# Kernel optimization log

Measured on AMD Instinct MI355X. Metric: run time of the kernel, lower is better.

The kernel has to match this reference:

```python
import jax, jax.numpy as jnp
import numpy as np

N_EXPERTS = 8
TOP_K = 2
AUX_COEF = 0.01
Z_COEF = 0.001


def setup_inputs() -> dict:
    key = jax.random.key(0)
    ks = jax.random.split(key, 5)
    B, S, D, F, E = 2, 2048, 768, 2048, N_EXPERTS
    std = 0.02
    std_out = std / np.sqrt(2 * 12)  # scale_init_by_depth, n_layers=12
    return {
        "x": jax.random.normal(ks[0], (B, S, D), jnp.float32),
        "router_w": jax.random.normal(ks[1], (D, E), jnp.float32) * std,
        "w1": jax.random.normal(ks[2], (E, D, F), jnp.float32) * std,
        "w2": jax.random.normal(ks[3], (E, F, D), jnp.float32) * std_out,
        "w3": jax.random.normal(ks[4], (E, D, F), jnp.float32) * std,
    }


def reference(x, router_w, w1, w2, w3):
    B, S, D = x.shape
    E = w1.shape[0]
    x_flat = x.reshape(-1, D)                      # [N, D]
    n_tokens = x_flat.shape[0]

    router_logits = x_flat @ router_w               # [N, E]
    probs = jax.nn.softmax(router_logits.astype(jnp.float32), axis=-1)
    topk_w, topk_i = jax.lax.top_k(probs, TOP_K)    # [N, K]
    topk_w = topk_w / jnp.sum(topk_w, axis=-1, keepdims=True)

    # Combine: equivalent to sort/group dispatch + per-expert GEMM + index_add,
    # expressed as a masked per-expert (fixed, small E) dense pass.
    out = jnp.zeros((n_tokens, D), dtype=x.dtype)
    for e in range(E):
        gate = jnp.sum(jnp.where(topk_i == e, topk_w, 0.0), axis=-1)  # [N] f32
        h = jax.nn.silu(x_flat @ w1[e]) * (x_flat @ w3[e])            # [N, F]
        out = out + gate[:, None].astype(x.dtype) * (h @ w2[e])

    # Switch-style load-balancing aux loss + z-loss
    importance = probs.mean(axis=0)                 # [E]
    top1 = topk_i[:, 0]
    load = jnp.zeros((E,), jnp.float32).at[top1].add(1.0) / n_tokens
    aux_loss = E * jnp.sum(importance * load) * AUX_COEF
    z_loss = jnp.mean(router_logits.astype(jnp.float32) ** 2) * Z_COEF

    return out.reshape(B, S, D), aux_loss, z_loss
```

## Files before the change

kernel.cpp:

```cpp
#include <hip/hip_runtime.h>
#include <hip/hip_bf16.h>

constexpr int NT = 4096;
constexpr int DD = 768;
constexpr int FF = 2048;
constexpr int NE = 8;
constexpr int MAXROWS = 9216;
constexpr int MAXMT128 = 72;
constexpr int MAXMT256 = 40;
constexpr int NKT1 = DD / 64;

constexpr int IDX_CNTA   = 0;
constexpr int IDX_CNTT1  = 8;
constexpr int IDX_CUR    = 16;
constexpr int IDX_IMP    = 24;
constexpr int IDX_ZSUM   = 32;
constexpr int IDX_NTILES = 33;
constexpr int IDX_OFF    = 34;
constexpr int IDX_EXPT   = 48;
constexpr int IDX_N256   = 120;
constexpr int IDX_E256   = 128;
constexpr int IDX_B256   = 168;
constexpr int IDX_L256   = 208;

constexpr size_t OFF_META   = 0;
constexpr size_t OFF_TKE    = 1024;
constexpr size_t OFF_GATE   = OFF_TKE    + (size_t)NT*2*4;
constexpr size_t OFF_ROWOF  = OFF_GATE   + (size_t)NT*2*4;
constexpr size_t OFF_TOKROW = OFF_ROWOF  + (size_t)NT*2*4;
constexpr size_t OFF_XG     = 136192;
constexpr size_t OFF_W1T    = OFF_XG  + (size_t)MAXROWS*DD*2;
constexpr size_t OFF_W3T    = OFF_W1T + (size_t)NE*FF*DD*2;
constexpr size_t OFF_W2T    = OFF_W3T + (size_t)NE*FF*DD*2;
constexpr size_t OFF_H      = OFF_W2T + (size_t)NE*FF*DD*2;
constexpr size_t OFF_OP     = OFF_H   + (size_t)MAXROWS*FF*2;

typedef float f32x4 __attribute__((ext_vector_type(4)));
typedef __bf16 bf16x8v __attribute__((ext_vector_type(8)));
typedef unsigned short u16x8 __attribute__((ext_vector_type(8)));

__device__ inline unsigned short f2bf_bits(float f) {
  __bf16 h = (__bf16)f;
  return *(unsigned short*)&h;
}
__device__ inline float bf2f(unsigned short u) {
  unsigned v = (unsigned)u << 16;
  return *(float*)&v;
}

__device__ __forceinline__ void glds16(const void* g, void* l) {
  __builtin_amdgcn_global_load_lds(
      (const __attribute__((address_space(1))) unsigned int*)g,
      (__attribute__((address_space(3))) unsigned int*)l, 16, 0, 0);
}

constexpr int RB = 128;
__global__ __launch_bounds__(256) void router_kernel(const float* __restrict__ x,
    const float* __restrict__ rw, int* __restrict__ meta,
    int* __restrict__ tke, float* __restrict__ gateArr) {
  __shared__ float s_imp[NE];
  __shared__ float s_z;
  __shared__ int s_cnt1[NE], s_cnta[NE];
  if (threadIdx.x < NE) { s_imp[threadIdx.x] = 0.f; s_cnt1[threadIdx.x] = 0; s_cnta[threadIdx.x] = 0; }
  if (threadIdx.x == 0) s_z = 0.f;
  __syncthreads();

  const int wave = threadIdx.x >> 6, lane = threadIdx.x & 63;
  float impacc[NE];
  #pragma unroll
  for (int e = 0; e < NE; ++e) impacc[e] = 0.f;
  float zacc = 0.f;

  for (int t = blockIdx.x * 4 + wave; t < NT; t += RB * 4) {
    float acc[NE];
    #pragma unroll
    for (int e = 0; e < NE; ++e) acc[e] = 0.f;
    const float* xr = x + (size_t)t * DD;
    for (int i = lane; i < DD; i += 64) {
      float xv = xr[i];
      const float* r = rw + i * NE;
      #pragma unroll
      for (int e = 0; e < NE; ++e) acc[e] += xv * r[e];
    }
    #pragma unroll
    for (int off = 32; off > 0; off >>= 1) {
      #pragma unroll
      for (int e = 0; e < NE; ++e) acc[e] += __shfl_xor(acc[e], off);
    }
    float mx = acc[0];
    #pragma unroll
    for (int e = 1; e < NE; ++e) mx = fmaxf(mx, acc[e]);
    float p[NE]; float s = 0.f;
    #pragma unroll
    for (int e = 0; e < NE; ++e) { p[e] = __expf(acc[e] - mx); s += p[e]; }
    float inv = 1.f / s;
    #pragma unroll
    for (int e = 0; e < NE; ++e) p[e] *= inv;
    int e0 = 0; float p0 = p[0];
    #pragma unroll
    for (int e = 1; e < NE; ++e) if (p[e] > p0) { p0 = p[e]; e0 = e; }
    int e1 = -1; float p1 = -1.f;
    #pragma unroll
    for (int e = 0; e < NE; ++e) if (e != e0 && p[e] > p1) { p1 = p[e]; e1 = e; }
    if (lane == 0) {
      #pragma unroll
      for (int e = 0; e < NE; ++e) { impacc[e] += p[e]; zacc += acc[e] * acc[e]; }
      atomicAdd(&s_cnt1[e0], 1);
      atomicAdd(&s_cnta[e0], 1);
      atomicAdd(&s_cnta[e1], 1);
      float gs = 1.f / (p0 + p1);
      tke[t*2]   = e0; tke[t*2+1] = e1;
      gateArr[t*2] = p0 * gs; gateArr[t*2+1] = p1 * gs;
    }
  }
  if (lane == 0) {
    #pragma unroll
    for (int e = 0; e < NE; ++e) atomicAdd(&s_imp[e], impacc[e]);
    atomicAdd(&s_z, zacc);
  }
  __syncthreads();
  float* fmeta = (float*)meta;
  if (threadIdx.x < NE) {
    atomicAdd(&fmeta[IDX_IMP + threadIdx.x], s_imp[threadIdx.x]);
    atomicAdd(&meta[IDX_CNTT1 + threadIdx.x], s_cnt1[threadIdx.x]);
    atomicAdd(&meta[IDX_CNTA + threadIdx.x], s_cnta[threadIdx.x]);
  }
  if (threadIdx.x == NE) atomicAdd(&fmeta[IDX_ZSUM], s_z);
}

__global__ __launch_bounds__(128) void scan_kernel(int* __restrict__ meta,
                                                   float* __restrict__ out_tail) {
  __shared__ int s_off[NE + 1];
  __shared__ int s_nt[NE];
  __shared__ float s_aux;
  const int t = threadIdx.x;
  if (t < NE) s_nt[t] = (meta[IDX_CNTA + t] + 127) >> 7;
  __syncthreads();
  if (t == 0) {
    int off = 0;
    for (int e = 0; e < NE; ++e) { s_off[e] = off; off += s_nt[e]; }
    s_off[NE] = off;
  }
  __syncthreads();
  const int ntiles = s_off[NE];
  if (t < NE) meta[IDX_OFF + t] = s_off[t] << 7;
  if (t == NE) { meta[IDX_OFF + NE] = ntiles << 7; meta[IDX_NTILES] = ntiles; }
  if (t < ntiles) {
    int e = 0;
    while (t >= s_off[e + 1]) e++;
    meta[IDX_EXPT + t] = e;
  }
  if (t == 0) {
    int n2t = 0;
    for (int e = 0; e < NE; ++e) {
      const int base = s_off[e] << 7;
      const int lim  = base + (s_nt[e] << 7);
      const int n2 = (s_nt[e] + 1) >> 1;
      for (int i = 0; i < n2; ++i) {
        meta[IDX_E256 + n2t] = e;
        meta[IDX_B256 + n2t] = base + (i << 8);
        meta[IDX_L256 + n2t] = lim;
        ++n2t;
      }
    }
    meta[IDX_N256] = n2t;
  }
  float* fmeta = (float*)meta;
  float pl = 0.f;
  if (t < NE)
    pl = (fmeta[IDX_IMP + t] / (float)NT) * ((float)meta[IDX_CNTT1 + t] / (float)NT);
  if (t < 64) {
    #pragma unroll
    for (int off = 4; off > 0; off >>= 1) pl += __shfl_xor(pl, off);
    if (t == 0) s_aux = pl;
  }
  __syncthreads();
  if (t == 0) {
    out_tail[0] = (float)NE * s_aux * 0.01f;
    out_tail[1] = fmeta[IDX_ZSUM] / (float)(NT * NE) * 0.001f;
  }
}

__global__ __launch_bounds__(256) void scatter_kernel(const int* __restrict__ tke,
    int* __restrict__ meta, int* __restrict__ rowof, int* __restrict__ tokrow) {
  __shared__ int s_cnt[NE], s_base[NE];
  const int t = blockIdx.x * 256 + threadIdx.x;
  if (threadIdx.x < NE) s_cnt[threadIdx.x] = 0;
  __syncthreads();
  const int e0 = tke[t*2], e1 = tke[t*2 + 1];
  const int l0 = atomicAdd(&s_cnt[e0], 1);
  const int l1 = atomicAdd(&s_cnt[e1], 1);
  __syncthreads();
  if (threadIdx.x < NE)
    s_base[threadIdx.x] = atomicAdd(&meta[IDX_CUR + threadIdx.x], s_cnt[threadIdx.x]);
  __syncthreads();
  const int r0 = meta[IDX_OFF + e0] + s_base[e0] + l0;
  const int r1 = meta[IDX_OFF + e1] + s_base[e1] + l1;
  rowof[t*2]     = r0;
  rowof[t*2 + 1] = r1;
  tokrow[r0] = t;
  tokrow[r1] = t;
}

__global__ __launch_bounds__(192) void gather_kernel(const float* __restrict__ x,
    const int* __restrict__ tokrow, const int* __restrict__ meta,
    __bf16* __restrict__ Xg) {
  const int row = blockIdx.x;
  if (row >= meta[IDX_OFF + NE]) return;
  const int tok = tokrow[row];
  ushort4* dst = (ushort4*)(Xg + (size_t)row * DD);
  const int i = threadIdx.x;
  ushort4 o;
  if (tok >= 0) {
    float4 v = ((const float4*)(x + (size_t)tok * DD))[i];
    o.x = f2bf_bits(v.x); o.y = f2bf_bits(v.y);
    o.z = f2bf_bits(v.z); o.w = f2bf_bits(v.w);
  } else {
    o.x = o.y = o.z = o.w = 0;
  }
  dst[i] = o;
}

constexpr int TS = 68;
__global__ __launch_bounds__(256) void transpose_cvt_all(
    const float* __restrict__ w1, const float* __restrict__ w3,
    const float* __restrict__ w2, __bf16* __restrict__ W1t,
    __bf16* __restrict__ W3t, __bf16* __restrict__ W2t) {
  const int z = blockIdx.z, which = z >> 3, e = z & 7;
  const float* src; __bf16* dst; int R, C, rt, ct;
  if (which == 0)      { src = w1; dst = W1t; R = DD; C = FF; rt = blockIdx.y; ct = blockIdx.x; }
  else if (which == 1) { src = w3; dst = W3t; R = DD; C = FF; rt = blockIdx.y; ct = blockIdx.x; }
  else                 { src = w2; dst = W2t; R = FF; C = DD; rt = blockIdx.x; ct = blockIdx.y; }
  src += (size_t)e * DD * FF; dst += (size_t)e * DD * FF;
  const int r0 = rt * 64, c0 = ct * 64;
  __shared__ __align__(16) __bf16 tile[64 * TS];
  const int t = threadIdx.x;
  #pragma unroll
  for (int i = 0; i < 4; ++i) {
    int idx = t + i * 256; int r = idx >> 4, q = idx & 15;
    float4 v = *(const float4*)&src[(size_t)(r0 + r) * C + c0 + q * 4];
    ushort4 o;
    o.x = f2bf_bits(v.x); o.y = f2bf_bits(v.y);
    o.z = f2bf_bits(v.z); o.w = f2bf_bits(v.w);
    *(ushort4*)&tile[r * TS + q * 4] = o;
  }
  __syncthreads();
  #pragma unroll
  for (int i = 0; i < 2; ++i) {
    int idx = t + i * 256; int c = idx >> 3, seg = idx & 7;
    u16x8 o;
    #pragma unroll
    for (int k = 0; k < 8; ++k)
      o[k] = *(unsigned short*)&tile[(seg * 8 + k) * TS + c];
    *(u16x8*)&dst[(size_t)(c0 + c) * R + r0 + seg * 8] = o;
  }
}

__global__ __launch_bounds__(512, 2) void gemm1_kernel(
    const __bf16* __restrict__ Xg, const __bf16* __restrict__ W1t,
    const __bf16* __restrict__ W3t, __bf16* __restrict__ Hb,
    const int* __restrict__ meta) {
  const int wgRaw = blockIdx.x + (int)gridDim.x * blockIdx.y;
  const int wg = (wgRaw & 7) * 80 + (wgRaw >> 3);
  const int mt = wg >> 4;
  const int n0 = (wg & 15) * 128;
  if (mt >= meta[IDX_N256]) return;
  const int e      = meta[IDX_E256 + mt];
  const int m0     = meta[IDX_B256 + mt];
  const int rowlim = meta[IDX_L256 + mt];

  __shared__ __align__(16) __bf16 As[2][256 * 64];
  __shared__ __align__(16) __bf16 Bs[2][256 * 64];

  const int t = threadIdx.x, lane = t & 63, wid = t >> 6;
  const int wm = wid >> 2, wn = wid & 3;
  const int lane15 = lane & 15, g = lane >> 4;

  const __bf16* __restrict__ W1e = W1t + (size_t)e * FF * DD;
  const __bf16* __restrict__ W3e = W3t + (size_t)e * FF * DD;

  const int aBase = (wm * 128 + lane15) * 64;
  const int bBase = (wn * 64 + lane15) * 64;
  const int c0 = ((g    ) ^ (lane & 7)) * 8;
  const int c1 = ((4 + g) ^ (lane & 7)) * 8;

  const int o0v = t, o1v = 512 + t;
  const int r0v = o0v >> 3, r1v = o1v >> 3;
  const int cl0 = (o0v & 7) ^ (r0v & 7), cl1 = (o1v & 7) ^ (r1v & 7);
  int gA00 = m0 + r0v;        if (gA00 >= MAXROWS) gA00 = 0;
  int gA01 = m0 + r1v;        if (gA01 >= MAXROWS) gA01 = 0;
  int gA10 = m0 + 128 + r0v;  if (gA10 >= MAXROWS) gA10 = 0;
  int gA11 = m0 + 128 + r1v;  if (gA11 >= MAXROWS) gA11 = 0;
  const __bf16* aS00 = Xg + (size_t)gA00 * DD + cl0 * 8;
  const __bf16* aS01 = Xg + (size_t)gA01 * DD + cl1 * 8;
  const __bf16* aS10 = Xg + (size_t)gA10 * DD + cl0 * 8;
  const __bf16* aS11 = Xg + (size_t)gA11 * DD + cl1 * 8;
  const int fc0 = n0 + ((r0v >> 5) << 4) + (r0v & 15);
  const int fc1 = n0 + ((r1v >> 5) << 4) + (r1v & 15);
  const __bf16* bW0 = (r0v & 16) ? W3e : W1e;
  const __bf16* bW1 = (r1v & 16) ? W3e : W1e;
  const __bf16* bS00 = bW0 + (size_t)fc0 * DD + cl0 * 8;
  const __bf16* bS01 = bW1 + (size_t)fc1 * DD + cl1 * 8;
  const __bf16* bS10 = bW0 + (size_t)(fc0 + 64) * DD + cl0 * 8;
  const __bf16* bS11 = bW1 + (size_t)(fc1 + 64) * DD + cl1 * 8;
  const int L00 = (       wid * 64) * 8;
  const int L01 = ( 512 + wid * 64) * 8;
  const int L10 = (1024 + wid * 64) * 8;
  const int L11 = (1536 + wid * 64) * 8;

  auto st2 = [&](__bf16* dstBuf, int kt, const __bf16* s0, const __bf16* s1,
                 int d0, int d1) {
    glds16(s0 + (size_t)kt * 64, dstBuf + d0);
    glds16(s1 + (size_t)kt * 64, dstBuf + d1);
  };

  const f32x4 zero = {0.f, 0.f, 0.f, 0.f};
  f32x4 acc[8][4];
  #pragma unroll
  for (int i = 0; i < 8; ++i)
    #pragma unroll
    for (int j = 0; j < 4; ++j) acc[i][j] = zero;

  __bf16 *Ac = &As[0][0], *An = &As[1][0];
  __bf16 *Bc = &Bs[0][0], *Bn = &Bs[1][0];

  st2(Ac, 0, aS00, aS01, L00, L01); st2(Ac, 0, aS10, aS11, L10, L11);
  st2(Bc, 0, bS00, bS01, L00, L01); st2(Bc, 0, bS10, bS11, L10, L11);
  st2(An, 1, aS00, aS01, L00, L01); st2(An, 1, aS10, aS11, L10, L11);
  st2(Bn, 1, bS00, bS01, L00, L01); st2(Bn, 1, bS10, bS11, L10, L11);
  asm volatile("s_waitcnt vmcnt(8)" ::: "memory");
  __builtin_amdgcn_s_barrier();

  bf16x8v af[8], ag[8], bf[8];

  for (int k = 0; k < NKT1; ++k) {
    const bool k2ok = (k < NKT1 - 2);
    #pragma unroll
    for (int i = 0; i < 4; ++i) {
      af[i*2+0] = *(const bf16x8v*)&Ac[aBase + i*1024 + c0];
      af[i*2+1] = *(const bf16x8v*)&Ac[aBase + i*1024 + c1];
    }
    #pragma unroll
    for (int j = 0; j < 4; ++j) {
      bf[j*2+0] = *(const bf16x8v*)&Bc[bBase + j*1024 + c0];
      bf[j*2+1] = *(const bf16x8v*)&Bc[bBase + j*1024 + c1];
    }
    __builtin_amdgcn_s_barrier();
    asm volatile("s_waitcnt lgkmcnt(0)" ::: "memory");
    __builtin_amdgcn_s_setprio(1);
    #pragma unroll
    for (int i = 0; i < 4; ++i)
      #pragma unroll
      for (int j = 0; j < 2; ++j) {
        acc[i][j] = __builtin_amdgcn_mfma_f32_16x16x32_bf16(af[i*2+0], bf[j*2+0], acc[i][j], 0, 0, 0);
        acc[i][j] = __builtin_amdgcn_mfma_f32_16x16x32_bf16(af[i*2+1], bf[j*2+1], acc[i][j], 0, 0, 0);
      }
    __builtin_amdgcn_s_setprio(0);
    __builtin_amdgcn_s_barrier();

    #pragma unroll
    for (int i = 0; i < 4; ++i) {
      ag[i*2+0] = *(const bf16x8v*)&Ac[aBase + (4+i)*1024 + c0];
      ag[i*2+1] = *(const bf16x8v*)&Ac[aBase + (4+i)*1024 + c1];
    }
    if (k2ok) st2(Bc, k + 2, bS00, bS01, L00, L01);
    __builtin_amdgcn_s_barrier();
    asm volatile("s_waitcnt lgkmcnt(0)" ::: "memory");
    __builtin_amdgcn_s_setprio(1);
    #pragma unroll
    for (int i = 0; i < 4; ++i)
      #pragma unroll
      for (int j = 0; j < 2; ++j) {
        acc[4+i][j] = __builtin_amdgcn_mfma_f32_16x16x32_bf16(ag[i*2+0], bf[j*2+0], acc[4+i][j], 0, 0, 0);
        acc[4+i][j] = __builtin_amdgcn_mfma_f32_16x16x32_bf16(ag[i*2+1], bf[j*2+1], acc[4+i][j], 0, 0, 0);
      }
    __builtin_amdgcn_s_setprio(0);
    __builtin_amdgcn_s_barrier();

    if (k2ok) {
      st2(Ac, k + 2, aS00, aS01, L00, L01);
      st2(Bc, k + 2, bS10, bS11, L10, L11);
    }
    __builtin_amdgcn_s_barrier();
    __builtin_amdgcn_s_setprio(1);
    #pragma unroll
    for (int i = 0; i < 4; ++i)
      #pragma unroll
      for (int j = 0; j < 2; ++j) {
        acc[i][2+j] = __builtin_amdgcn_mfma_f32_16x16x32_bf16(af[i*2+0], bf[(2+j)*2+0], acc[i][2+j], 0, 0, 0);
        acc[i][2+j] = __builtin_amdgcn_mfma_f32_16x16x32_bf16(af[i*2+1], bf[(2+j)*2+1], acc[i][2+j], 0, 0, 0);
      }
    __builtin_amdgcn_s_setprio(0);
    __builtin_amdgcn_s_barrier();

    if (k2ok) st2(Ac, k + 2, aS10, aS11, L10, L11);
    __builtin_amdgcn_s_barrier();
    __builtin_amdgcn_s_setprio(1);
    #pragma unroll
    for (int i = 0; i < 4; ++i)
      #pragma unroll
      for (int j = 0; j < 2; ++j) {
        acc[4+i][2+j] = __builtin_amdgcn_mfma_f32_16x16x32_bf16(ag[i*2+0], bf[(2+j)*2+0], acc[4+i][2+j], 0, 0, 0);
        acc[4+i][2+j] = __builtin_amdgcn_mfma_f32_16x16x32_bf16(ag[i*2+1], bf[(2+j)*2+1], acc[4+i][2+j], 0, 0, 0);
      }
    __builtin_amdgcn_s_setprio(0);
    if (k2ok)               { asm volatile("s_waitcnt vmcnt(8)" ::: "memory"); }
    else if (k == NKT1 - 2) { asm volatile("s_waitcnt vmcnt(0)" ::: "memory"); }
    __builtin_amdgcn_s_barrier();

    __bf16* tp;
    tp = Ac; Ac = An; An = tp;
    tp = Bc; Bc = Bn; Bn = tp;
  }

  #pragma unroll
  for (int i = 0; i < 8; ++i) {
    const int grow = m0 + wm * 128 + i * 16 + (lane >> 4) * 4;
    #pragma unroll
    for (int p = 0; p < 2; ++p) {
      const int col = n0 + (wn * 2 + p) * 16 + lane15;
      const f32x4 v1 = acc[i][2*p], v3 = acc[i][2*p + 1];
      #pragma unroll
      for (int r = 0; r < 4; ++r) {
        if (grow + r < rowlim) {
          float h = v1[r] / (1.f + __expf(-v1[r])) * v3[r];
          Hb[(size_t)(grow + r) * FF + col] = (__bf16)h;
        }
      }
    }
  }
}

__global__ __launch_bounds__(256) void gemm2_kernel(const __bf16* __restrict__ Hb,
    const __bf16* __restrict__ W2t, __bf16* __restrict__ OP,
    const int* __restrict__ meta) {
  const int mt = blockIdx.y;
  if (mt >= meta[IDX_NTILES]) return;
  const int e = meta[IDX_EXPT + mt];
  const int n0 = blockIdx.x * 128;
  const int m0 = mt * 128;
  __shared__ __align__(16) __bf16 As[128*32], Bs[128*32];
  const int t = threadIdx.x, wave = t >> 6, lane = t & 63;
  const int wm = wave & 1, wn = wave >> 1;
  const __bf16* w2e = W2t + (size_t)e * DD * FF;
  const f32x4 zero = {0.f, 0.f, 0.f, 0.f};
  f32x4 acc[4][4];
  #pragma unroll
  for (int i = 0; i < 4; ++i)
    #pragma unroll
    for (int j = 0; j < 4; ++j) acc[i][j] = zero;

  const __bf16* gA = Hb  + (size_t)(m0 + 32*wave + (lane >> 2)) * FF + (lane & 3) * 8;
  const __bf16* gB = w2e + (size_t)(n0 + 32*wave + (lane >> 2)) * FF + (lane & 3) * 8;
  __bf16* lA0 = &As[(32*wave     ) * 32];
  __bf16* lA1 = &As[(32*wave + 16) * 32];
  __bf16* lB0 = &Bs[(32*wave     ) * 32];
  __bf16* lB1 = &Bs[(32*wave + 16) * 32];

  for (int k0 = 0; k0 < FF; k0 += 32) {
    glds16(gA + k0,          lA0);
    glds16(gA + k0 + 16*FF,  lA1);
    glds16(gB + k0,          lB0);
    glds16(gB + k0 + 16*FF,  lB1);
    __syncthreads();
    bf16x8v a[4], b[4];
    #pragma unroll
    for (int i = 0; i < 4; ++i) {
      a[i] = *(const bf16x8v*)&As[(64*wm + 16*i + (lane & 15))*32 + (lane >> 4)*8];
      b[i] = *(const bf16x8v*)&Bs[(64*wn + 16*i + (lane & 15))*32 + (lane >> 4)*8];
    }
    #pragma unroll
    for (int i = 0; i < 4; ++i)
      #pragma unroll
      for (int j = 0; j < 4; ++j)
        acc[i][j] = __builtin_amdgcn_mfma_f32_16x16x32_bf16(a[i], b[j], acc[i][j], 0, 0, 0);
    __syncthreads();
  }
  #pragma unroll
  for (int i = 0; i < 4; ++i) {
    const int rowb = m0 + 64*wm + 16*i + (lane >> 4)*4;
    #pragma unroll
    for (int j = 0; j < 4; ++j) {
      const int col = n0 + 64*wn + 16*j + (lane & 15);
      #pragma unroll
      for (int r = 0; r < 4; ++r)
        OP[(size_t)(rowb + r)*DD + col] = (__bf16)acc[i][j][r];
    }
  }
}

__global__ __launch_bounds__(192) void combine_kernel(const __bf16* __restrict__ OP,
    const int* __restrict__ rowof, const float* __restrict__ gateArr,
    float* __restrict__ out) {
  const int t = blockIdx.x;
  const int r0 = rowof[t*2], r1 = rowof[t*2 + 1];
  const float g0 = gateArr[t*2], g1 = gateArr[t*2 + 1];
  const ushort4* p0 = (const ushort4*)(OP + (size_t)r0 * DD);
  const ushort4* p1 = (const ushort4*)(OP + (size_t)r1 * DD);
  const int i = threadIdx.x;
  ushort4 a = p0[i], b = p1[i];
  float4 o;
  o.x = g0 * bf2f(a.x) + g1 * bf2f(b.x);
  o.y = g0 * bf2f(a.y) + g1 * bf2f(b.y);
  o.z = g0 * bf2f(a.z) + g1 * bf2f(b.z);
  o.w = g0 * bf2f(a.w) + g1 * bf2f(b.w);
  ((float4*)(out + (size_t)t * DD))[i] = o;
}

extern "C" void kernel_launch(void* const* d_in, const int* in_sizes, int n_in,
                              void* d_out, int out_size, void* d_ws, size_t ws_size,
                              hipStream_t stream) {
  const float* x  = (const float*)d_in[0];
  const float* rw = (const float*)d_in[1];
  const float* w1 = (const float*)d_in[2];
  const float* w2 = (const float*)d_in[3];
  const float* w3 = (const float*)d_in[4];
  float* out = (float*)d_out;

  char* ws = (char*)d_ws;
  int*    meta   = (int*)(ws + OFF_META);
  int*    tke    = (int*)(ws + OFF_TKE);
  float*  gateA  = (float*)(ws + OFF_GATE);
  int*    rowof  = (int*)(ws + OFF_ROWOF);
  int*    tokrow = (int*)(ws + OFF_TOKROW);
  __bf16* Xg     = (__bf16*)(ws + OFF_XG);
  __bf16* W1t    = (__bf16*)(ws + OFF_W1T);
  __bf16* W3t    = (__bf16*)(ws + OFF_W3T);
  __bf16* W2t    = (__bf16*)(ws + OFF_W2T);
  __bf16* Hb     = (__bf16*)(ws + OFF_H);
  __bf16* OP     = (__bf16*)(ws + OFF_OP);

  hipMemsetAsync(ws + OFF_META, 0, 1024, stream);
  hipMemsetAsync(ws + OFF_TOKROW, 0xFF, (size_t)MAXROWS * 4, stream);

  transpose_cvt_all<<<dim3(32, 12, 24), 256, 0, stream>>>(w1, w3, w2, W1t, W3t, W2t);

  router_kernel<<<RB, 256, 0, stream>>>(x, rw, meta, tke, gateA);
  scan_kernel<<<1, 128, 0, stream>>>(meta, out + (size_t)NT * DD);
  scatter_kernel<<<NT/256, 256, 0, stream>>>(tke, meta, rowof, tokrow);
  gather_kernel<<<MAXROWS, 192, 0, stream>>>(x, tokrow, meta, Xg);

  gemm1_kernel<<<dim3(FF/128, MAXMT256), 512, 0, stream>>>(Xg, W1t, W3t, Hb, meta);
  gemm2_kernel<<<dim3(DD/128, MAXMT128), 256, 0, stream>>>(Hb, W2t, OP, meta);
  combine_kernel<<<NT, 192, 0, stream>>>(OP, rowof, gateA, out);
}
```

Baseline: 393.1 us.

## Make gemm1 persistent with atomic work-queue tile scheduling

```diff
diff --git a/kernel.cpp b/kernel.cpp
--- a/kernel.cpp
+++ b/kernel.cpp
@@ -22,6 +22,7 @@
 constexpr int IDX_E256   = 128;
 constexpr int IDX_B256   = 168;
 constexpr int IDX_L256   = 208;
+constexpr int IDX_WORK   = 250;
 
 constexpr size_t OFF_META   = 0;
 constexpr size_t OFF_TKE    = 1024;
@@ -259,172 +260,185 @@
 __global__ __launch_bounds__(512, 2) void gemm1_kernel(
     const __bf16* __restrict__ Xg, const __bf16* __restrict__ W1t,
     const __bf16* __restrict__ W3t, __bf16* __restrict__ Hb,
-    const int* __restrict__ meta) {
-  const int wgRaw = blockIdx.x + (int)gridDim.x * blockIdx.y;
-  const int wg = (wgRaw & 7) * 80 + (wgRaw >> 3);
-  const int mt = wg >> 4;
-  const int n0 = (wg & 15) * 128;
-  if (mt >= meta[IDX_N256]) return;
-  const int e      = meta[IDX_E256 + mt];
-  const int m0     = meta[IDX_B256 + mt];
-  const int rowlim = meta[IDX_L256 + mt];
-
+    int* __restrict__ meta) {
   __shared__ __align__(16) __bf16 As[2][256 * 64];
   __shared__ __align__(16) __bf16 Bs[2][256 * 64];
+  __shared__ int s_wi;
 
   const int t = threadIdx.x, lane = t & 63, wid = t >> 6;
   const int wm = wid >> 2, wn = wid & 3;
   const int lane15 = lane & 15, g = lane >> 4;
 
-  const __bf16* __restrict__ W1e = W1t + (size_t)e * FF * DD;
-  const __bf16* __restrict__ W3e = W3t + (size_t)e * FF * DD;
-
   const int aBase = (wm * 128 + lane15) * 64;
-  const int bBase = (wn * 64 + lane15) * 64;
+  const int bBase = (wn * 32 + lane15) * 64;
   const int c0 = ((g    ) ^ (lane & 7)) * 8;
   const int c1 = ((4 + g) ^ (lane & 7)) * 8;
 
   const int o0v = t, o1v = 512 + t;
   const int r0v = o0v >> 3, r1v = o1v >> 3;
   const int cl0 = (o0v & 7) ^ (r0v & 7), cl1 = (o1v & 7) ^ (r1v & 7);
-  int gA00 = m0 + r0v;        if (gA00 >= MAXROWS) gA00 = 0;
-  int gA01 = m0 + r1v;        if (gA01 >= MAXROWS) gA01 = 0;
-  int gA10 = m0 + 128 + r0v;  if (gA10 >= MAXROWS) gA10 = 0;
-  int gA11 = m0 + 128 + r1v;  if (gA11 >= MAXROWS) gA11 = 0;
-  const __bf16* aS00 = Xg + (size_t)gA00 * DD + cl0 * 8;
-  const __bf16* aS01 = Xg + (size_t)gA01 * DD + cl1 * 8;
-  const __bf16* aS10 = Xg + (size_t)gA10 * DD + cl0 * 8;
-  const __bf16* aS11 = Xg + (size_t)gA11 * DD + cl1 * 8;
-  const int fc0 = n0 + ((r0v >> 5) << 4) + (r0v & 15);
-  const int fc1 = n0 + ((r1v >> 5) << 4) + (r1v & 15);
-  const __bf16* bW0 = (r0v & 16) ? W3e : W1e;
-  const __bf16* bW1 = (r1v & 16) ? W3e : W1e;
-  const __bf16* bS00 = bW0 + (size_t)fc0 * DD + cl0 * 8;
-  const __bf16* bS01 = bW1 + (size_t)fc1 * DD + cl1 * 8;
-  const __bf16* bS10 = bW0 + (size_t)(fc0 + 64) * DD + cl0 * 8;
-  const __bf16* bS11 = bW1 + (size_t)(fc1 + 64) * DD + cl1 * 8;
   const int L00 = (       wid * 64) * 8;
   const int L01 = ( 512 + wid * 64) * 8;
   const int L10 = (1024 + wid * 64) * 8;
   const int L11 = (1536 + wid * 64) * 8;
-
-  auto st2 = [&](__bf16* dstBuf, int kt, const __bf16* s0, const __bf16* s1,
-                 int d0, int d1) {
-    glds16(s0 + (size_t)kt * 64, dstBuf + d0);
-    glds16(s1 + (size_t)kt * 64, dstBuf + d1);
-  };
-
-  const f32x4 zero = {0.f, 0.f, 0.f, 0.f};
-  f32x4 acc[8][4];
-  #pragma unroll
-  for (int i = 0; i < 8; ++i)
-    #pragma unroll
-    for (int j = 0; j < 4; ++j) acc[i][j] = zero;
-
-  __bf16 *Ac = &As[0][0], *An = &As[1][0];
-  __bf16 *Bc = &Bs[0][0], *Bn = &Bs[1][0];
-
-  st2(Ac, 0, aS00, aS01, L00, L01); st2(Ac, 0, aS10, aS11, L10, L11);
-  st2(Bc, 0, bS00, bS01, L00, L01); st2(Bc, 0, bS10, bS11, L10, L11);
-  st2(An, 1, aS00, aS01, L00, L01); st2(An, 1, aS10, aS11, L10, L11);
-  st2(Bn, 1, bS00, bS01, L00, L01); st2(Bn, 1, bS10, bS11, L10, L11);
-  asm volatile("s_waitcnt vmcnt(8)" ::: "memory");
-  __builtin_amdgcn_s_barrier();
-
-  bf16x8v af[8], ag[8], bf[8];
-
-  for (int k = 0; k < NKT1; ++k) {
-    const bool k2ok = (k < NKT1 - 2);
-    #pragma unroll
-    for (int i = 0; i < 4; ++i) {
-      af[i*2+0] = *(const bf16x8v*)&Ac[aBase + i*1024 + c0];
-      af[i*2+1] = *(const bf16x8v*)&Ac[aBase + i*1024 + c1];
-    }
-    #pragma unroll
-    for (int j = 0; j < 4; ++j) {
-      bf[j*2+0] = *(const bf16x8v*)&Bc[bBase + j*1024 + c0];
-      bf[j*2+1] = *(const bf16x8v*)&Bc[bBase + j*1024 + c1];
-    }
+  const int fcb0 = ((r0v >> 5) << 4) + (r0v & 15);
+  const int fcb1 = ((r1v >> 5) << 4) + (r1v & 15);
+  const bool w3sel0 = (r0v & 16) != 0, w3sel1 = (r1v & 16) != 0;
+
+  const int nItems = meta[IDX_N256] * 16;
+
+  while (true) {
+    if (t == 0) s_wi = atomicAdd(&meta[IDX_WORK], 1);
+    __syncthreads();
+    const int wi = s_wi;
+    if (wi >= nItems) return;
+    const int mt = wi >> 4;
+    const int n0 = (wi & 15) * 128;
+    const int e      = meta[IDX_E256 + mt];
+    const int m0     = meta[IDX_B256 + mt];
+    const int rowlim = meta[IDX_L256 + mt];
+
+    const __bf16* __restrict__ W1e = W1t + (size_t)e * FF * DD;
+    const __bf16* __restrict__ W3e = W3t + (size_t)e * FF * DD;
+
+    int gA00 = m0 + r0v;        if (gA00 >= MAXROWS) gA00 = 0;
+    int gA01 = m0 + r1v;        if (gA01 >= MAXROWS) gA01 = 0;
+    int gA10 = m0 + 128 + r0v;  if (gA10 >= MAXROWS) gA10 = 0;
+    int gA11 = m0 + 128 + r1v;  if (gA11 >= MAXROWS) gA11 = 0;
+    const __bf16* aS00 = Xg + (size_t)gA00 * DD + cl0 * 8;
+    const __bf16* aS01 = Xg + (size_t)gA01 * DD + cl1 * 8;
+    const __bf16* aS10 = Xg + (size_t)gA10 * DD + cl0 * 8;
+    const __bf16* aS11 = Xg + (size_t)gA11 * DD + cl1 * 8;
+    const __bf16* bW0 = w3sel0 ? W3e : W1e;
+    const __bf16* bW1 = w3sel1 ? W3e : W1e;
+    const __bf16* bS00 = bW0 + (size_t)(n0 + fcb0) * DD + cl0 * 8;
+    const __bf16* bS01 = bW1 + (size_t)(n0 + fcb1) * DD + cl1 * 8;
+    const __bf16* bS10 = bW0 + (size_t)(n0 + fcb0 + 64) * DD + cl0 * 8;
+    const __bf16* bS11 = bW1 + (size_t)(n0 + fcb1 + 64) * DD + cl1 * 8;
+
+    auto st2 = [&](__bf16* dstBuf, int kt, const __bf16* s0, const __bf16* s1,
+                   int d0, int d1) {
+      glds16(s0 + (size_t)kt * 64, dstBuf + d0);
+      glds16(s1 + (size_t)kt * 64, dstBuf + d1);
+    };
+
+    const f32x4 zero = {0.f, 0.f, 0.f, 0.f};
+    f32x4 acc[8][4];
+    #pragma unroll
+    for (int i = 0; i < 8; ++i)
+      #pragma unroll
+      for (int j = 0; j < 4; ++j) acc[i][j] = zero;
+
+    __bf16 *Ac = &As[0][0], *An = &As[1][0];
+    __bf16 *Bc = &Bs[0][0], *Bn = &Bs[1][0];
+
+    st2(Ac, 0, aS00, aS01, L00, L01); st2(Ac, 0, aS10, aS11, L10, L11);
+    st2(Bc, 0, bS00, bS01, L00, L01); st2(Bc, 0, bS10, bS11, L10, L11);
+    st2(An, 1, aS00, aS01, L00, L01); st2(An, 1, aS10, aS11, L10, L11);
+    st2(Bn, 1, bS00, bS01, L00, L01); st2(Bn, 1, bS10, bS11, L10, L11);
+    asm volatile("s_waitcnt vmcnt(8)" ::: "memory");
     __builtin_amdgcn_s_barrier();
-    asm volatile("s_waitcnt lgkmcnt(0)" ::: "memory");
-    __builtin_amdgcn_s_setprio(1);
-    #pragma unroll
-    for (int i = 0; i < 4; ++i)
+
+    bf16x8v af[8], ag[8], bfr[8];
+
+    for (int k = 0; k < NKT1; ++k) {
+      const bool k2ok = (k < NKT1 - 2);
+      #pragma unroll
+      for (int i = 0; i < 4; ++i) {
+        af[i*2+0] = *(const bf16x8v*)&Ac[aBase + i*1024 + c0];
+        af[i*2+1] = *(const bf16x8v*)&Ac[aBase + i*1024 + c1];
+      }
       #pragma unroll
       for (int j = 0; j < 2; ++j) {
-        acc[i][j] = __builtin_amdgcn_mfma_f32_16x16x32_bf16(af[i*2+0], bf[j*2+0], acc[i][j], 0, 0, 0);
-        acc[i][j] = __builtin_amdgcn_mfma_f32_16x16x32_bf16(af[i*2+1], bf[j*2+1], acc[i][j], 0, 0, 0);
-      }
-    __builtin_amdgcn_s_setprio(0);
-    __builtin_amdgcn_s_barrier();
-
-    #pragma unroll
-    for (int i = 0; i < 4; ++i) {
-      ag[i*2+0] = *(const bf16x8v*)&Ac[aBase + (4+i)*1024 + c0];
-      ag[i*2+1] = *(const bf16x8v*)&Ac[aBase + (4+i)*1024 + c1];
-    }
-    if (k2ok) st2(Bc, k + 2, bS00, bS01, L00, L01);
-    __builtin_amdgcn_s_barrier();
-    asm volatile("s_waitcnt lgkmcnt(0)" ::: "memory");
-    __builtin_amdgcn_s_setprio(1);
-    #pragma unroll
-    for (int i = 0; i < 4; ++i)
+        bfr[j*2+0] = *(const bf16x8v*)&Bc[bBase + j*1024 + c0];
+        bfr[j*2+1] = *(const bf16x8v*)&Bc[bBase + j*1024 + c1];
+      }
+      __builtin_amdgcn_s_barrier();
+      asm volatile("s_waitcnt lgkmcnt(0)" ::: "memory");
+      __builtin_amdgcn_s_setprio(1);
+      #pragma unroll
+      for (int i = 0; i < 4; ++i)
+        #pragma unroll
+        for (int j = 0; j < 2; ++j) {
+          acc[i][j] = __builtin_amdgcn_mfma_f32_16x16x32_bf16(af[i*2+0], bfr[j*2+0], acc[i][j], 0, 0, 0);
+          acc[i][j] = __builtin_amdgcn_mfma_f32_16x16x32_bf16(af[i*2+1], bfr[j*2+1], acc[i][j], 0, 0, 0);
+        }
+      __builtin_amdgcn_s_setprio(0);
+      __builtin_amdgcn_s_barrier();
+
+      #pragma unroll
+      for (int i = 0; i < 4; ++i) {
+        ag[i*2+0] = *(const bf16x8v*)&Ac[aBase + (4+i)*1024 + c0];
+        ag[i*2+1] = *(const bf16x8v*)&Ac[aBase + (4+i)*1024 + c1];
+      }
       #pragma unroll
       for (int j = 0; j < 2; ++j) {
-        acc[4+i][j] = __builtin_amdgcn_mfma_f32_16x16x32_bf16(ag[i*2+0], bf[j*2+0], acc[4+i][j], 0, 0, 0);
-        acc[4+i][j] = __builtin_amdgcn_mfma_f32_16x16x32_bf16(ag[i*2+1], bf[j*2+1], acc[4+i][j], 0, 0, 0);
-      }
-    __builtin_amdgcn_s_setprio(0);
-    __builtin_amdgcn_s_barrier();
-
-    if (k2ok) {
-      st2(Ac, k + 2, aS00, aS01, L00, L01);
-      st2(Bc, k + 2, bS10, bS11, L10, L11);
-    }
-    __builtin_amdgcn_s_barrier();
-    __builtin_amdgcn_s_setprio(1);
-    #pragma unroll
-    for (int i = 0; i < 4; ++i)
-      #pragma unroll
-      for (int j = 0; j < 2; ++j) {
-        acc[i][2+j] = __builtin_amdgcn_mfma_f32_16x16x32_bf16(af[i*2+0], bf[(2+j)*2+0], acc[i][2+j], 0, 0, 0);
-        acc[i][2+j] = __builtin_amdgcn_mfma_f32_16x16x32_bf16(af[i*2+1], bf[(2+j)*2+1], acc[i][2+j], 0, 0, 0);
-      }
-    __builtin_amdgcn_s_setprio(0);
-    __builtin_amdgcn_s_barrier();
-
-    if (k2ok) st2(Ac, k + 2, aS10, aS11, L10, L11);
-    __builtin_amdgcn_s_barrier();
-    __builtin_amdgcn_s_setprio(1);
-    #pragma unroll
-    for (int i = 0; i < 4; ++i)
-      #pragma unroll
-      for (int j = 0; j < 2; ++j) {
-        acc[4+i][2+j] = __builtin_amdgcn_mfma_f32_16x16x32_bf16(ag[i*2+0], bf[(2+j)*2+0], acc[4+i][2+j], 0, 0, 0);
-        acc[4+i][2+j] = __builtin_amdgcn_mfma_f32_16x16x32_bf16(ag[i*2+1], bf[(2+j)*2+1], acc[4+i][2+j], 0, 0, 0);
-      }
-    __builtin_amdgcn_s_setprio(0);
-    if (k2ok)               { asm volatile("s_waitcnt vmcnt(8)" ::: "memory"); }
-    else if (k == NKT1 - 2) { asm volatile("s_waitcnt vmcnt(0)" ::: "memory"); }
-    __builtin_amdgcn_s_barrier();
-
-    __bf16* tp;
-    tp = Ac; Ac = An; An = tp;
-    tp = Bc; Bc = Bn; Bn = tp;
-  }
-
-  #pragma unroll
-  for (int i = 0; i < 8; ++i) {
-    const int grow = m0 + wm * 128 + i * 16 + (lane >> 4) * 4;
-    #pragma unroll
-    for (int p = 0; p < 2; ++p) {
-      const int col = n0 + (wn * 2 + p) * 16 + lane15;
-      const f32x4 v1 = acc[i][2*p], v3 = acc[i][2*p + 1];
-      #pragma unroll
-      for (int r = 0; r < 4; ++r) {
-        if (grow + r < rowlim) {
-          float h = v1[r] / (1.f + __expf(-v1[r])) * v3[r];
-          Hb[(size_t)(grow + r) * FF + col] = (__bf16)h;
+        bfr[4+j*2+0] = *(const bf16x8v*)&Bc[bBase + 8192 + j*1024 + c0];
+        bfr[4+j*2+1] = *(const bf16x8v*)&Bc[bBase + 8192 + j*1024 + c1];
+      }
+      if (k2ok) st2(Bc, k + 2, bS00, bS01, L00, L01);
+      __builtin_amdgcn_s_barrier();
+      asm volatile("s_waitcnt lgkmcnt(0)" ::: "memory");
+      __builtin_amdgcn_s_setprio(1);
+      #pragma unroll
+      for (int i = 0; i < 4; ++i)
+        #pragma unroll
+        for (int j = 0; j < 2; ++j) {
+          acc[4+i][j] = __builtin_amdgcn_mfma_f32_16x16x32_bf16(ag[i*2+0], bfr[j*2+0], acc[4+i][j], 0, 0, 0);
+          acc[4+i][j] = __builtin_amdgcn_mfma_f32_16x16x32_bf16(ag[i*2+1], bfr[j*2+1], acc[4+i][j], 0, 0, 0);
+        }
+      __builtin_amdgcn_s_setprio(0);
+      __builtin_amdgcn_s_barrier();
+
+      if (k2ok) {
+        st2(Ac, k + 2, aS00, aS01, L00, L01);
+        st2(Bc, k + 2, bS10, bS11, L10, L11);
+      }
+      __builtin_amdgcn_s_barrier();
+      __builtin_amdgcn_s_setprio(1);
+      #pragma unroll
+      for (int i = 0; i < 4; ++i)
+        #pragma unroll
+        for (int j = 0; j < 2; ++j) {
+          acc[i][2+j] = __builtin_amdgcn_mfma_f32_16x16x32_bf16(af[i*2+0], bfr[4+j*2+0], acc[i][2+j], 0, 0, 0);
+          acc[i][2+j] = __builtin_amdgcn_mfma_f32_16x16x32_bf16(af[i*2+1], bfr[4+j*2+1], acc[i][2+j], 0, 0, 0);
+        }
+      __builtin_amdgcn_s_setprio(0);
+      __builtin_amdgcn_s_barrier();
+
+      if (k2ok) st2(Ac, k + 2, aS10, aS11, L10, L11);
+      __builtin_amdgcn_s_barrier();
+      __builtin_amdgcn_s_setprio(1);
+      #pragma unroll
+      for (int i = 0; i < 4; ++i)
+        #pragma unroll
+        for (int j = 0; j < 2; ++j) {
+          acc[4+i][2+j] = __builtin_amdgcn_mfma_f32_16x16x32_bf16(ag[i*2+0], bfr[4+j*2+0], acc[4+i][2+j], 0, 0, 0);
+          acc[4+i][2+j] = __builtin_amdgcn_mfma_f32_16x16x32_bf16(ag[i*2+1], bfr[4+j*2+1], acc[4+i][2+j], 0, 0, 0);
+        }
+      __builtin_amdgcn_s_setprio(0);
+      if (k2ok)               { asm volatile("s_waitcnt vmcnt(8)" ::: "memory"); }
+      else if (k == NKT1 - 2) { asm volatile("s_waitcnt vmcnt(0)" ::: "memory"); }
+      __builtin_amdgcn_s_barrier();
+
+      __bf16* tp;
+      tp = Ac; Ac = An; An = tp;
+      tp = Bc; Bc = Bn; Bn = tp;
+    }
+
+    #pragma unroll
+    for (int i = 0; i < 8; ++i) {
+      const int grow = m0 + wm * 128 + i * 16 + (lane >> 4) * 4;
+      #pragma unroll
+      for (int p = 0; p < 2; ++p) {
+        const int col = n0 + (wn + p * 4) * 16 + lane15;
+        const f32x4 v1 = acc[i][2*p], v3 = acc[i][2*p + 1];
+        #pragma unroll
+        for (int r = 0; r < 4; ++r) {
+          if (grow + r < rowlim) {
+            float h = v1[r] / (1.f + __expf(-v1[r])) * v3[r];
+            Hb[(size_t)(grow + r) * FF + col] = (__bf16)h;
+          }
         }
       }
     }
@@ -540,7 +554,7 @@
   scatter_kernel<<<NT/256, 256, 0, stream>>>(tke, meta, rowof, tokrow);
   gather_kernel<<<MAXROWS, 192, 0, stream>>>(x, tokrow, meta, Xg);
 
-  gemm1_kernel<<<dim3(FF/128, MAXMT256), 512, 0, stream>>>(Xg, W1t, W3t, Hb, meta);
+  gemm1_kernel<<<dim3(256), 512, 0, stream>>>(Xg, W1t, W3t, Hb, meta);
   gemm2_kernel<<<dim3(DD/128, MAXMT128), 256, 0, stream>>>(Hb, W2t, OP, meta);
   combine_kernel<<<NT, 192, 0, stream>>>(OP, rowof, gateA, out);
 }
```

Measured after the change: 407.8 us. 3.7% more time.

## Rewrite gemm2 as 256x128 double-buffered LDS-pipelined MFMA kernel over 256-row tiles

Applied to the files above, without the earlier changes.

```diff
diff --git a/kernel.cpp b/kernel.cpp
--- a/kernel.cpp
+++ b/kernel.cpp
@@ -9,6 +9,7 @@
 constexpr int MAXMT128 = 72;
 constexpr int MAXMT256 = 40;
 constexpr int NKT1 = DD / 64;
+constexpr int NKT2 = FF / 64;
 
 constexpr int IDX_CNTA   = 0;
 constexpr int IDX_CNTT1  = 8;
@@ -260,14 +261,12 @@
     const __bf16* __restrict__ Xg, const __bf16* __restrict__ W1t,
     const __bf16* __restrict__ W3t, __bf16* __restrict__ Hb,
     const int* __restrict__ meta) {
-  const int wgRaw = blockIdx.x + (int)gridDim.x * blockIdx.y;
-  const int wg = (wgRaw & 7) * 80 + (wgRaw >> 3);
-  const int mt = wg >> 4;
-  const int n0 = (wg & 15) * 128;
+  const int mt = blockIdx.y;
   if (mt >= meta[IDX_N256]) return;
   const int e      = meta[IDX_E256 + mt];
   const int m0     = meta[IDX_B256 + mt];
   const int rowlim = meta[IDX_L256 + mt];
+  const int n0 = blockIdx.x * 128;
 
   __shared__ __align__(16) __bf16 As[2][256 * 64];
   __shared__ __align__(16) __bf16 Bs[2][256 * 64];
@@ -431,60 +430,136 @@
   }
 }
 
-__global__ __launch_bounds__(256) void gemm2_kernel(const __bf16* __restrict__ Hb,
-    const __bf16* __restrict__ W2t, __bf16* __restrict__ OP,
-    const int* __restrict__ meta) {
+__global__ __launch_bounds__(512, 2) void gemm2_kernel(
+    const __bf16* __restrict__ Hb, const __bf16* __restrict__ W2t,
+    __bf16* __restrict__ OP, const int* __restrict__ meta) {
   const int mt = blockIdx.y;
-  if (mt >= meta[IDX_NTILES]) return;
-  const int e = meta[IDX_EXPT + mt];
+  if (mt >= meta[IDX_N256]) return;
+  const int e      = meta[IDX_E256 + mt];
+  const int m0     = meta[IDX_B256 + mt];
+  const int rowlim = meta[IDX_L256 + mt];
   const int n0 = blockIdx.x * 128;
-  const int m0 = mt * 128;
-  __shared__ __align__(16) __bf16 As[128*32], Bs[128*32];
-  const int t = threadIdx.x, wave = t >> 6, lane = t & 63;
-  const int wm = wave & 1, wn = wave >> 1;
-  const __bf16* w2e = W2t + (size_t)e * DD * FF;
+
+  __shared__ __align__(16) __bf16 As[2][256 * 64];
+  __shared__ __align__(16) __bf16 Bs[2][128 * 64];
+
+  const int t = threadIdx.x, lane = t & 63, wid = t >> 6;
+  const int wm = wid >> 2, wn = wid & 3;
+  const int lane15 = lane & 15, g = lane >> 4;
+
+  const __bf16* __restrict__ W2e = W2t + (size_t)e * DD * FF;
+
+  const int aBase = (wm * 128 + lane15) * 64;
+  const int bBase = (wn * 32 + lane15) * 64;
+  const int c0 = ((g    ) ^ (lane & 7)) * 8;
+  const int c1 = ((4 + g) ^ (lane & 7)) * 8;
+
+  const int o0v = t, o1v = 512 + t;
+  const int r0v = o0v >> 3, r1v = o1v >> 3;
+  const int cl0 = (o0v & 7) ^ (r0v & 7), cl1 = (o1v & 7) ^ (r1v & 7);
+  const int L00 = (       wid * 64) * 8;
+  const int L01 = ( 512 + wid * 64) * 8;
+  const int L10 = (1024 + wid * 64) * 8;
+  const int L11 = (1536 + wid * 64) * 8;
+
+  int gA00 = m0 + r0v;        if (gA00 >= MAXROWS) gA00 = 0;
+  int gA01 = m0 + r1v;        if (gA01 >= MAXROWS) gA01 = 0;
+  int gA10 = m0 + 128 + r0v;  if (gA10 >= MAXROWS) gA10 = 0;
+  int gA11 = m0 + 128 + r1v;  if (gA11 >= MAXROWS) gA11 = 0;
+  const __bf16* aS00 = Hb + (size_t)gA00 * FF + cl0 * 8;
+  const __bf16* aS01 = Hb + (size_t)gA01 * FF + cl1 * 8;
+  const __bf16* aS10 = Hb + (size_t)gA10 * FF + cl0 * 8;
+  const __bf16* aS11 = Hb + (size_t)gA11 * FF + cl1 * 8;
+  const __bf16* bS0  = W2e + (size_t)(n0 + r0v) * FF + cl0 * 8;
+  const __bf16* bS1  = W2e + (size_t)(n0 + r1v) * FF + cl1 * 8;
+
+  auto stA = [&](__bf16* d, int kt) {
+    glds16(aS00 + (size_t)kt * 64, d + L00);
+    glds16(aS01 + (size_t)kt * 64, d + L01);
+    glds16(aS10 + (size_t)kt * 64, d + L10);
+    glds16(aS11 + (size_t)kt * 64, d + L11);
+  };
+  auto stB = [&](__bf16* d, int kt) {
+    glds16(bS0 + (size_t)kt * 64, d + L00);
+    glds16(bS1 + (size_t)kt * 64, d + L01);
+  };
+
   const f32x4 zero = {0.f, 0.f, 0.f, 0.f};
-  f32x4 acc[4][4];
+  f32x4 acc[8][2];
   #pragma unroll
-  for (int i = 0; i < 4; ++i)
-    #pragma unroll
-    for (int j = 0; j < 4; ++j) acc[i][j] = zero;
-
-  const __bf16* gA = Hb  + (size_t)(m0 + 32*wave + (lane >> 2)) * FF + (lane & 3) * 8;
-  const __bf16* gB = w2e + (size_t)(n0 + 32*wave + (lane >> 2)) * FF + (lane & 3) * 8;
-  __bf16* lA0 = &As[(32*wave     ) * 32];
-  __bf16* lA1 = &As[(32*wave + 16) * 32];
-  __bf16* lB0 = &Bs[(32*wave     ) * 32];
-  __bf16* lB1 = &Bs[(32*wave + 16) * 32];
-
-  for (int k0 = 0; k0 < FF; k0 += 32) {
-    glds16(gA + k0,          lA0);
-    glds16(gA + k0 + 16*FF,  lA1);
-    glds16(gB + k0,          lB0);
-    glds16(gB + k0 + 16*FF,  lB1);
-    __syncthreads();
-    bf16x8v a[4], b[4];
+  for (int i = 0; i < 8; ++i)
+    #pragma unroll
+    for (int j = 0; j < 2; ++j) acc[i][j] = zero;
+
+  __bf16 *Ac = &As[0][0], *An = &As[1][0];
+  __bf16 *Bc = &Bs[0][0], *Bn = &Bs[1][0];
+
+  stA(Ac, 0); stB(Bc, 0);
+  stA(An, 1); stB(Bn, 1);
+  asm volatile("s_waitcnt vmcnt(6)" ::: "memory");
+  __builtin_amdgcn_s_barrier();
+
+  bf16x8v af[8], ag[8], bfr[4];
+
+  for (int k = 0; k < NKT2; ++k) {
+    const bool k2ok = (k < NKT2 - 2);
     #pragma unroll
     for (int i = 0; i < 4; ++i) {
-      a[i] = *(const bf16x8v*)&As[(64*wm + 16*i + (lane & 15))*32 + (lane >> 4)*8];
-      b[i] = *(const bf16x8v*)&Bs[(64*wn + 16*i + (lane & 15))*32 + (lane >> 4)*8];
-    }
+      af[i*2+0] = *(const bf16x8v*)&Ac[aBase + i*1024 + c0];
+      af[i*2+1] = *(const bf16x8v*)&Ac[aBase + i*1024 + c1];
+    }
+    #pragma unroll
+    for (int i = 0; i < 4; ++i) {
+      ag[i*2+0] = *(const bf16x8v*)&Ac[aBase + (4+i)*1024 + c0];
+      ag[i*2+1] = *(const bf16x8v*)&Ac[aBase + (4+i)*1024 + c1];
+    }
+    #pragma unroll
+    for (int j = 0; j < 2; ++j) {
+      bfr[j*2+0] = *(const bf16x8v*)&Bc[bBase + j*1024 + c0];
+      bfr[j*2+1] = *(const bf16x8v*)&Bc[bBase + j*1024 + c1];
+    }
+    __builtin_amdgcn_s_barrier();
+    asm volatile("s_waitcnt lgkmcnt(0)" ::: "memory");
+    __builtin_amdgcn_s_setprio(1);
     #pragma unroll
     for (int i = 0; i < 4; ++i)
       #pragma unroll
-      for (int j = 0; j < 4; ++j)
-        acc[i][j] = __builtin_amdgcn_mfma_f32_16x16x32_bf16(a[i], b[j], acc[i][j], 0, 0, 0);
-    __syncthreads();
-  }
+      for (int j = 0; j < 2; ++j) {
+        acc[i][j] = __builtin_amdgcn_mfma_f32_16x16x32_bf16(af[i*2+0], bfr[j*2+0], acc[i][j], 0, 0, 0);
+        acc[i][j] = __builtin_amdgcn_mfma_f32_16x16x32_bf16(af[i*2+1], bfr[j*2+1], acc[i][j], 0, 0, 0);
+      }
+    __builtin_amdgcn_s_setprio(0);
+    __builtin_amdgcn_s_barrier();
+
+    if (k2ok) { stA(Ac, k + 2); stB(Bc, k + 2); }
+    __builtin_amdgcn_s_setprio(1);
+    #pragma unroll
+    for (int i = 0; i < 4; ++i)
+      #pragma unroll
+      for (int j = 0; j < 2; ++j) {
+        acc[4+i][j] = __builtin_amdgcn_mfma_f32_16x16x32_bf16(ag[i*2+0], bfr[j*2+0], acc[4+i][j], 0, 0, 0);
+        acc[4+i][j] = __builtin_amdgcn_mfma_f32_16x16x32_bf16(ag[i*2+1], bfr[j*2+1], acc[4+i][j], 0, 0, 0);
+      }
+    __builtin_amdgcn_s_setprio(0);
+    if (k2ok)               { asm volatile("s_waitcnt vmcnt(6)" ::: "memory"); }
+    else if (k == NKT2 - 2) { asm volatile("s_waitcnt vmcnt(0)" ::: "memory"); }
+    __builtin_amdgcn_s_barrier();
+
+    __bf16* tp;
+    tp = Ac; Ac = An; An = tp;
+    tp = Bc; Bc = Bn; Bn = tp;
+  }
+
   #pragma unroll
-  for (int i = 0; i < 4; ++i) {
-    const int rowb = m0 + 64*wm + 16*i + (lane >> 4)*4;
-    #pragma unroll
-    for (int j = 0; j < 4; ++j) {
-      const int col = n0 + 64*wn + 16*j + (lane & 15);
+  for (int i = 0; i < 8; ++i) {
+    const int rowb = m0 + wm * 128 + i * 16 + (lane >> 4) * 4;
+    #pragma unroll
+    for (int jj = 0; jj < 2; ++jj) {
+      const int col = n0 + wn * 32 + jj * 16 + lane15;
       #pragma unroll
       for (int r = 0; r < 4; ++r)
-        OP[(size_t)(rowb + r)*DD + col] = (__bf16)acc[i][j][r];
+        if (rowb + r < rowlim)
+          OP[(size_t)(rowb + r) * DD + col] = (__bf16)acc[i][jj][r];
     }
   }
 }
@@ -541,6 +616,6 @@
   gather_kernel<<<MAXROWS, 192, 0, stream>>>(x, tokrow, meta, Xg);
 
   gemm1_kernel<<<dim3(FF/128, MAXMT256), 512, 0, stream>>>(Xg, W1t, W3t, Hb, meta);
-  gemm2_kernel<<<dim3(DD/128, MAXMT128), 256, 0, stream>>>(Hb, W2t, OP, meta);
+  gemm2_kernel<<<dim3(DD/128, MAXMT256), 512, 0, stream>>>(Hb, W2t, OP, meta);
   combine_kernel<<<NT, 192, 0, stream>>>(OP, rowof, gateA, out);
 }
```

New measurement: 391.3 us. No clear change (-0.5%).
